# Performance work log

Measured on AMD Instinct MI355X. Metric: run time of the kernel, lower is better.

The kernel has to match this reference:

```python
import jax, jax.numpy as jnp
import numpy as np

NUM_CHANNELS = 64  # d per group
T_ITERS = 5
EPS = 1e-05


def setup_inputs() -> dict:
    key = jax.random.key(0)
    kx, = jax.random.split(key, 1)
    X = jax.random.normal(kx, (64, 256, 56, 56), dtype=jnp.float32)
    weight = jnp.ones((1, 256, 1, 1), dtype=jnp.float32)
    bias = jnp.zeros((1, 256, 1, 1), dtype=jnp.float32)
    return {"X": X, "weight": weight, "bias": bias}


def reference(X, weight, bias):
    B, C, H, W = X.shape
    nc = NUM_CHANNELS
    g = C // nc
    # (C, B, H, W) -> (g, nc, m) with m = B*H*W
    x = jnp.transpose(X, (1, 0, 2, 3)).reshape(g, nc, -1)
    m = x.shape[-1]
    mean = x.mean(-1, keepdims=True)                      # (g, nc, 1)
    xc = x - mean
    I = jnp.broadcast_to(jnp.eye(nc, dtype=X.dtype), (g, nc, nc))
    # Sigma = eps*I + (1/m) * xc @ xc^T
    Sigma = EPS * I + jnp.einsum('gdm,gem->gde', xc, xc) / m
    # rTr = 1 / trace(Sigma) per group
    rTr = (1.0 / jnp.einsum('gii->g', Sigma))[:, None, None]  # (g,1,1)
    Sigma_N = Sigma * rTr
    # Newton-Schulz iteration: P <- 1.5*P - 0.5*P^3 @ Sigma_N
    P = I
    for _ in range(T_ITERS):
        P3 = jnp.einsum('gij,gjk,gkl->gil', P, P, P)
        P = 1.5 * P - 0.5 * jnp.einsum('gij,gjk->gik', P3, Sigma_N)
    wm = P * jnp.sqrt(rTr)                                 # whitening matrix (g, nc, nc)
    xn = jnp.einsum('gde,gem->gdm', wm, xc)                # whitened data
    X_hat = jnp.transpose(xn.reshape(C, B, H, W), (1, 0, 2, 3))
    return X_hat * weight + bias
```

## Files before the change

kernel.cpp:

```cpp
#include <hip/hip_runtime.h>
#include <hip/hip_bf16.h>
#include <math.h>


#define EPS_F 1e-5f

using f32x4v = __attribute__((ext_vector_type(4))) float;
using f32x2v = __attribute__((ext_vector_type(2))) float;
using short8 = __attribute__((ext_vector_type(8))) short;
using u32x4  = __attribute__((ext_vector_type(4))) unsigned int;

constexpr int Cc  = 256;
constexpr int HWc = 3136;
constexpr int CHW = Cc * HWc;
constexpr float Mf = 200704.0f;
constexpr int GX  = 196;
constexpr int LDB = 72;

constexpr int WS_SUM  = 0;
constexpr int WS_G    = 256;
constexpr int WS_WM   = WS_G + 16384;
constexpr int WS_BETA = WS_WM + 16384;
constexpr int WS_SLAB = WS_BETA + 256;
constexpr int WS_SSUM = WS_SLAB + 784 * 4096;

__device__ __forceinline__ unsigned cvtpk(float lo, float hi) {
    __hip_bfloat162 h = __float22bfloat162_rn(float2{lo, hi});
    unsigned u;
    __builtin_memcpy(&u, &h, 4);
    return u;
}

__device__ __forceinline__ f32x4v mfma16(short8 a, short8 b, f32x4v c) {
    return __builtin_amdgcn_mfma_f32_16x16x32_bf16(a, b, c, 0, 0, 0);
}

extern "C" __global__ __launch_bounds__(256, 4)
void k_gram(const float* __restrict__ X, float* __restrict__ ws) {
    __shared__ __align__(16) unsigned short tg[2][2][64 * LDB];
    const int g = blockIdx.y, bx = blockIdx.x, tid = threadIdx.x;
    const int lane = tid & 63, w = tid >> 6;
    const int row = tid >> 2, mo = (tid & 3) << 4;
    const int l15 = lane & 15, lg = lane >> 4;
    const int CBi0 = (w >> 1) << 1, CBj0 = (w & 1) << 1;
    const float* Xg = X + (size_t)g * 64 * HWc;

    f32x4v acc[2][2];
    #pragma unroll
    for (int i = 0; i < 2; ++i)
        #pragma unroll
        for (int j = 0; j < 2; ++j) acc[i][j] = (f32x4v){0.f, 0.f, 0.f, 0.f};
    float csum = 0.0f;

    f32x4v curA[4], curB[4];
    auto loadt = [&](int t, f32x4v* cur) {
        const int b = t / 49, hw0 = (t - b * 49) << 6;
        const float* p = Xg + (size_t)b * CHW + (size_t)row * HWc + hw0 + mo;
        cur[0] = *(const f32x4v*)(p);      cur[1] = *(const f32x4v*)(p + 4);
        cur[2] = *(const f32x4v*)(p + 8);  cur[3] = *(const f32x4v*)(p + 12);
    };
    auto packt = [&](const f32x4v* cur, unsigned short* dstbuf) {
        unsigned pk[8];
        #pragma unroll
        for (int i = 0; i < 4; ++i) {
            csum += (cur[i].x + cur[i].y) + (cur[i].z + cur[i].w);
            pk[2*i]   = cvtpk(cur[i].x, cur[i].y);
            pk[2*i+1] = cvtpk(cur[i].z, cur[i].w);
        }
        unsigned short* dst = dstbuf + row * LDB + mo;
        *(u32x4*)(dst)     = (u32x4){pk[0], pk[1], pk[2], pk[3]};
        *(u32x4*)(dst + 8) = (u32x4){pk[4], pk[5], pk[6], pk[7]};
    };
    auto comp = [&](const unsigned short* T) {
        #pragma unroll
        for (int s = 0; s < 2; ++s) {
            const int ko = 8 * lg + 32 * s;
            const short8 a0 = *(const short8*)&T[(CBi0 * 16      + l15) * LDB + ko];
            const short8 a1 = *(const short8*)&T[((CBi0+1) * 16  + l15) * LDB + ko];
            const short8 b0 = *(const short8*)&T[(CBj0 * 16      + l15) * LDB + ko];
            const short8 b1 = *(const short8*)&T[((CBj0+1) * 16  + l15) * LDB + ko];
            acc[0][0] = mfma16(a0, b0, acc[0][0]);
            acc[0][1] = mfma16(a0, b1, acc[0][1]);
            acc[1][0] = mfma16(a1, b0, acc[1][0]);
            acc[1][1] = mfma16(a1, b1, acc[1][1]);
        }
    };

    loadt(bx, curA);
    loadt(bx + GX, curB);

    int buf = 0;
    for (int kk = 0; kk < 8; ++kk) {
        packt(curA, tg[buf][0]);
        packt(curB, tg[buf][1]);
        __syncthreads();
        if (kk < 7) {
            loadt(bx + GX * (2*kk + 2), curA);
            loadt(bx + GX * (2*kk + 3), curB);
        }
        comp(tg[buf][0]);
        comp(tg[buf][1]);
        buf ^= 1;
    }

    csum += __shfl_down(csum, 1, 4);
    csum += __shfl_down(csum, 2, 4);
    if ((tid & 3) == 0)
        ws[WS_SSUM + (g * GX + bx) * 64 + row] = csum;

    float* Gp = ws + WS_SLAB + (size_t)(g * GX + bx) * 4096;
    #pragma unroll
    for (int ci = 0; ci < 2; ++ci)
        #pragma unroll
        for (int cj = 0; cj < 2; ++cj)
            #pragma unroll
            for (int reg = 0; reg < 4; ++reg) {
                const int r = (CBi0 + ci) * 16 + lg * 4 + reg;
                const int c = (CBj0 + cj) * 16 + l15;
                Gp[r * 64 + c] = acc[ci][cj][reg];
            }
}

extern "C" __global__ __launch_bounds__(256)
void k_reduce(float* __restrict__ ws) {
    const int g = blockIdx.y, chunk = blockIdx.x, tid = threadIdx.x;
    const int cell = chunk * 256 + tid;
    const float* p = ws + WS_SLAB + (size_t)g * GX * 4096 + cell;
    float s0 = 0.f, s1 = 0.f, s2 = 0.f, s3 = 0.f;
    #pragma unroll 7
    for (int s4 = 0; s4 < 49; ++s4) {
        s0 += p[0];
        s1 += p[4096];
        s2 += p[2 * 4096];
        s3 += p[3 * 4096];
        p += 4 * 4096;
    }
    ws[WS_G + g * 4096 + cell] = (s0 + s1) + (s2 + s3);

    if (chunk == 0 && tid < 64) {
        const float* q = ws + WS_SSUM + (size_t)g * GX * 64 + tid;
        float a0 = 0.f, a1 = 0.f, a2 = 0.f, a3 = 0.f;
        #pragma unroll 7
        for (int s4 = 0; s4 < 49; ++s4) {
            a0 += q[0];
            a1 += q[64];
            a2 += q[128];
            a3 += q[192];
            q += 256;
        }
        ws[WS_SUM + g * 64 + tid] = (a0 + a1) + (a2 + a3);
    }
}

__device__ __forceinline__
void mm64s(float* C, const float* A, const float* B, int r0, int c0) {
    f32x4v s[4] = {{0,0,0,0},{0,0,0,0},{0,0,0,0},{0,0,0,0}};
    #pragma unroll 4
    for (int kk = 0; kk < 16; ++kk) {
        const f32x4v b0 = *(const f32x4v*)&B[(4*kk + 0) * 68 + c0];
        const f32x4v b1 = *(const f32x4v*)&B[(4*kk + 1) * 68 + c0];
        const f32x4v b2 = *(const f32x4v*)&B[(4*kk + 2) * 68 + c0];
        const f32x4v b3 = *(const f32x4v*)&B[(4*kk + 3) * 68 + c0];
        #pragma unroll
        for (int i = 0; i < 4; ++i) {
            const f32x4v a = *(const f32x4v*)&A[(r0 + i) * 68 + 4 * kk];
            s[i] += a.x * b0 + a.y * b1 + a.z * b2 + a.w * b3;
        }
    }
    __syncthreads();
    #pragma unroll
    for (int i = 0; i < 4; ++i) *(f32x4v*)&C[(r0 + i) * 68 + c0] = s[i];
    __syncthreads();
}

extern "C" __global__ __launch_bounds__(256)
void k_solve(const float* __restrict__ weight, const float* __restrict__ bias,
             float* __restrict__ ws) {
    __shared__ __align__(16) float M [64 * 68];
    __shared__ __align__(16) float P [64 * 68];
    __shared__ __align__(16) float W [64 * 68];
    __shared__ __align__(16) float T1[64 * 68];
    __shared__ __align__(16) float mean_s[64];
    __shared__ float red;

    const int g = blockIdx.x, tid = threadIdx.x;
    const int r = tid >> 2, ch = (tid & 3) << 4;
    const int r0 = (tid >> 4) << 2, c0 = (tid & 15) << 2;

    if (tid < 64) mean_s[tid] = ws[WS_SUM + g * 64 + tid] * (1.0f / Mf);
    __syncthreads();

    const float* Gp = ws + WS_G + g * 4096;
    const float mr = mean_s[r];
    #pragma unroll
    for (int j4 = 0; j4 < 4; ++j4) {
        const int c = ch + 4 * j4;
        const f32x4v gv = *(const f32x4v*)&Gp[r * 64 + c];
        const f32x4v mc = *(const f32x4v*)&mean_s[c];
        f32x4v sv, pv = {0,0,0,0};
        #pragma unroll
        for (int j = 0; j < 4; ++j) {
            float v = gv[j] * (1.0f / Mf) - mr * mc[j];
            if (c + j == r) { v += EPS_F; pv[j] = 1.0f; }
            sv[j] = v;
        }
        *(f32x4v*)&M[r * 68 + c] = sv;
        *(f32x4v*)&P[r * 68 + c] = pv;
    }
    __syncthreads();

    if (tid == 0) {
        float tr = 0.f;
        #pragma unroll
        for (int i = 0; i < 64; ++i) tr += M[i * 68 + i];
        red = 1.0f / tr;
    }
    __syncthreads();
    const float rtr = red;
    #pragma unroll
    for (int j4 = 0; j4 < 4; ++j4) {
        const int c = ch + 4 * j4;
        *(f32x4v*)&M[r * 68 + c] = *(const f32x4v*)&M[r * 68 + c] * rtr;
    }
    __syncthreads();

    for (int t = 0; t < 5; ++t) {
        #pragma unroll
        for (int j4 = 0; j4 < 4; ++j4) {
            const int c = ch + 4 * j4;
            f32x4v mv = *(const f32x4v*)&M[r * 68 + c];
            f32x4v wv = -0.5f * mv;
            #pragma unroll
            for (int j = 0; j < 4; ++j) if (c + j == r) wv[j] += 1.5f;
            *(f32x4v*)&W[r * 68 + c] = wv;
        }
        __syncthreads();
        mm64s(P, P, W, r0, c0);
        if (t < 4) {
            mm64s(T1, M, W, r0, c0);
            mm64s(M, T1, W, r0, c0);
        }
    }

    const float srtr = sqrtf(rtr);
    const float wr = weight[g * 64 + r];
    float* Wp = ws + WS_WM + g * 4096;
    float part = 0.0f;
    #pragma unroll
    for (int j4 = 0; j4 < 4; ++j4) {
        const int c = ch + 4 * j4;
        const f32x4v pv = *(const f32x4v*)&P[r * 68 + c] * srtr;
        *(f32x4v*)&Wp[r * 64 + c] = pv * wr;
        const f32x4v mc = *(const f32x4v*)&mean_s[c];
        part += pv.x * mc.x + pv.y * mc.y + pv.z * mc.z + pv.w * mc.w;
    }
    part += __shfl_down(part, 1, 4);
    part += __shfl_down(part, 2, 4);
    if ((tid & 3) == 0)
        ws[WS_BETA + g * 64 + r] = bias[g * 64 + r] - wr * part;
}

extern "C" __global__ __launch_bounds__(256, 4)
void k_apply(const float* __restrict__ X, const float* __restrict__ ws,
             float* __restrict__ out) {
    __shared__ __align__(16) unsigned short tx[2][2][64 * LDB];
    __shared__ __align__(16) float beta_sh[64];

    const int g = blockIdx.y, bx = blockIdx.x, tid = threadIdx.x;
    const int lane = tid & 63, w = tid >> 6;
    const int l15 = lane & 15, lg = lane >> 4;
    const float* Xg = X + (size_t)g * 64 * HWc;

    {
        unsigned short* wm_s = &tx[0][0][0];
        const float* Wp = ws + WS_WM + g * 4096;
        const int r = tid >> 2, ch = (tid & 3) << 4;
        const float* p = Wp + r * 64 + ch;
        const f32x4v v0 = *(const f32x4v*)(p);      const f32x4v v1 = *(const f32x4v*)(p + 4);
        const f32x4v v2 = *(const f32x4v*)(p + 8);  const f32x4v v3 = *(const f32x4v*)(p + 12);
        unsigned short* dst = &wm_s[r * LDB + ch];
        *(u32x4*)(dst)     = (u32x4){cvtpk(v0.x,v0.y), cvtpk(v0.z,v0.w),
                                     cvtpk(v1.x,v1.y), cvtpk(v1.z,v1.w)};
        *(u32x4*)(dst + 8) = (u32x4){cvtpk(v2.x,v2.y), cvtpk(v2.z,v2.w),
                                     cvtpk(v3.x,v3.y), cvtpk(v3.z,v3.w)};
        if (tid < 64) beta_sh[tid] = ws[WS_BETA + g * 64 + tid];
    }
    __syncthreads();

    const int CB0 = (w >> 1) << 1, MB0 = (w & 1) << 1;
    short8 afrag[2][2];
    {
        const unsigned short* wm_s = &tx[0][0][0];
        #pragma unroll
        for (int ci = 0; ci < 2; ++ci)
            #pragma unroll
            for (int s = 0; s < 2; ++s)
                afrag[ci][s] = *(const short8*)&wm_s[((CB0 + ci) * 16 + l15) * LDB + 8 * lg + 32 * s];
    }

    float betav[2][4]; int crow[2][4];
    #pragma unroll
    for (int ci = 0; ci < 2; ++ci)
        #pragma unroll
        for (int reg = 0; reg < 4; ++reg) {
            const int cl = (CB0 + ci) * 16 + lg * 4 + reg;
            betav[ci][reg] = beta_sh[cl];
            crow[ci][reg]  = (g * 64 + cl) * HWc;
        }
    __syncthreads();

    const int rT   = 32 * (lane >> 5) + 16 * (lane & 1) + ((lane & 31) >> 1);
    const int mcb  = 32 * (w & 1) + 2 * l15;
    const int e0 = w * 16;

    float curA[16], curB[16];
    auto loadt = [&](int t, float* cur) {
        const int b = t / 49, hw0 = (t - b * 49) << 6;
        const float* p = Xg + (size_t)b * CHW + (size_t)e0 * HWc + hw0 + lane;
        #pragma unroll
        for (int j = 0; j < 16; ++j) cur[j] = p[(size_t)j * HWc];
    };
    auto packt = [&](const float* cur, unsigned short* dstbuf) {
        unsigned short* dst = dstbuf + rT * LDB + e0;
        *(u32x4*)(dst)     = (u32x4){cvtpk(cur[0],cur[1]),   cvtpk(cur[2],cur[3]),
                                     cvtpk(cur[4],cur[5]),   cvtpk(cur[6],cur[7])};
        *(u32x4*)(dst + 8) = (u32x4){cvtpk(cur[8],cur[9]),   cvtpk(cur[10],cur[11]),
                                     cvtpk(cur[12],cur[13]), cvtpk(cur[14],cur[15])};
    };
    auto compst = [&](const unsigned short* T, int t) {
        f32x4v acc[2][2];
        #pragma unroll
        for (int i = 0; i < 2; ++i)
            #pragma unroll
            for (int j = 0; j < 2; ++j) acc[i][j] = (f32x4v){0.f,0.f,0.f,0.f};
        #pragma unroll
        for (int s = 0; s < 2; ++s) {
            const int ko = 8 * lg + 32 * s;
            const short8 b0 = *(const short8*)&T[(MB0 * 16     + l15) * LDB + ko];
            const short8 b1 = *(const short8*)&T[((MB0+1) * 16 + l15) * LDB + ko];
            acc[0][0] = mfma16(afrag[0][s], b0, acc[0][0]);
            acc[0][1] = mfma16(afrag[0][s], b1, acc[0][1]);
            acc[1][0] = mfma16(afrag[1][s], b0, acc[1][0]);
            acc[1][1] = mfma16(afrag[1][s], b1, acc[1][1]);
        }
        const int b = t / 49, hw0 = (t - b * 49) << 6;
        float* ob = out + (size_t)b * CHW + hw0 + mcb;
        #pragma unroll
        for (int ci = 0; ci < 2; ++ci)
            #pragma unroll
            for (int reg = 0; reg < 4; ++reg) {
                const float bt = betav[ci][reg];
                const f32x2v v = {acc[ci][0][reg] + bt, acc[ci][1][reg] + bt};
                __builtin_nontemporal_store(v, (f32x2v*)(ob + crow[ci][reg]));
            }
    };

    loadt(bx, curA);
    loadt(bx + GX, curB);

    int buf = 0;
    for (int kk = 0; kk < 8; ++kk) {
        packt(curA, tx[buf][0]);
        packt(curB, tx[buf][1]);
        __syncthreads();
        if (kk < 7) {
            loadt(bx + GX * (2*kk + 2), curA);
            loadt(bx + GX * (2*kk + 3), curB);
        }
        compst(tx[buf][0], bx + GX * (2*kk));
        compst(tx[buf][1], bx + GX * (2*kk + 1));
        buf ^= 1;
    }
}

extern "C" void kernel_launch(void* const* d_in, const int* in_sizes, int n_in,
                              void* d_out, int out_size, void* d_ws, size_t ws_size,
                              hipStream_t stream) {
    const float* X      = (const float*)d_in[0];
    const float* weight = (const float*)d_in[1];
    const float* bias   = (const float*)d_in[2];
    float* out = (float*)d_out;
    float* ws  = (float*)d_ws;

    hipLaunchKernelGGL(k_gram,   dim3(GX, 4), dim3(256), 0, stream, X, ws);
    hipLaunchKernelGGL(k_reduce, dim3(16, 4), dim3(256), 0, stream, ws);
    hipLaunchKernelGGL(k_solve,  dim3(4),     dim3(256), 0, stream, weight, bias, ws);
    hipLaunchKernelGGL(k_apply,  dim3(GX, 4), dim3(256), 0, stream, X, ws, out);
}
```

Measured before the change: 153.5 us.

## Use split-bf16 MFMA for Newton-Schulz solve and widen slab reduction grid

The 64x64 fp32 matrix products in the Newton-Schulz solve were done with scalar FMAs from shared memory. They now run on bf16 MFMA instructions, with each operand split into high and low bf16 parts and three products summed to keep near-fp32 accuracy. Separately, the slab reduction now uses 4x more blocks, each splitting the 196 partial slabs across four waves and combining the results in shared memory. The goal is to cut the serial latency of the tiny single-block-per-group solve kernel and to give the reduction more parallelism. The cost is extra precision-splitting and conversion work, and slightly less accuracy than true fp32.

```diff
diff --git a/kernel.cpp b/kernel.cpp
--- a/kernel.cpp
+++ b/kernel.cpp
@@ -29,6 +29,16 @@
     unsigned u;
     __builtin_memcpy(&u, &h, 4);
     return u;
+}
+
+__device__ __forceinline__ unsigned short bf16rn(float v) {
+    unsigned u = __builtin_bit_cast(unsigned, v);
+    u += 0x7FFFu + ((u >> 16) & 1u);
+    return (unsigned short)(u >> 16);
+}
+__device__ __forceinline__ float frombf(unsigned short h) {
+    unsigned u = (unsigned)h << 16;
+    return __builtin_bit_cast(float, u);
 }
 
 __device__ __forceinline__ f32x4v mfma16(short8 a, short8 b, f32x4v c) {
@@ -123,122 +133,175 @@
 
 extern "C" __global__ __launch_bounds__(256)
 void k_reduce(float* __restrict__ ws) {
+    __shared__ float part[4][64];
     const int g = blockIdx.y, chunk = blockIdx.x, tid = threadIdx.x;
-    const int cell = chunk * 256 + tid;
-    const float* p = ws + WS_SLAB + (size_t)g * GX * 4096 + cell;
-    float s0 = 0.f, s1 = 0.f, s2 = 0.f, s3 = 0.f;
+    const int c63 = tid & 63, q = tid >> 6;
+    const float* p = ws + WS_SLAB + (size_t)g * GX * 4096
+                   + (size_t)(q * 49) * 4096 + chunk * 64 + c63;
+    float s = 0.f;
     #pragma unroll 7
-    for (int s4 = 0; s4 < 49; ++s4) {
-        s0 += p[0];
-        s1 += p[4096];
-        s2 += p[2 * 4096];
-        s3 += p[3 * 4096];
-        p += 4 * 4096;
-    }
-    ws[WS_G + g * 4096 + cell] = (s0 + s1) + (s2 + s3);
+    for (int i = 0; i < 49; ++i) { s += *p; p += 4096; }
+    part[q][c63] = s;
+    __syncthreads();
+    if (tid < 64)
+        ws[WS_G + g * 4096 + chunk * 64 + tid] =
+            (part[0][tid] + part[1][tid]) + (part[2][tid] + part[3][tid]);
 
     if (chunk == 0 && tid < 64) {
-        const float* q = ws + WS_SSUM + (size_t)g * GX * 64 + tid;
+        const float* qq = ws + WS_SSUM + (size_t)g * GX * 64 + tid;
         float a0 = 0.f, a1 = 0.f, a2 = 0.f, a3 = 0.f;
         #pragma unroll 7
         for (int s4 = 0; s4 < 49; ++s4) {
-            a0 += q[0];
-            a1 += q[64];
-            a2 += q[128];
-            a3 += q[192];
-            q += 256;
+            a0 += qq[0];
+            a1 += qq[64];
+            a2 += qq[128];
+            a3 += qq[192];
+            qq += 256;
         }
         ws[WS_SUM + g * 64 + tid] = (a0 + a1) + (a2 + a3);
     }
 }
 
-__device__ __forceinline__
-void mm64s(float* C, const float* A, const float* B, int r0, int c0) {
-    f32x4v s[4] = {{0,0,0,0},{0,0,0,0},{0,0,0,0},{0,0,0,0}};
-    #pragma unroll 4
-    for (int kk = 0; kk < 16; ++kk) {
-        const f32x4v b0 = *(const f32x4v*)&B[(4*kk + 0) * 68 + c0];
-        const f32x4v b1 = *(const f32x4v*)&B[(4*kk + 1) * 68 + c0];
-        const f32x4v b2 = *(const f32x4v*)&B[(4*kk + 2) * 68 + c0];
-        const f32x4v b3 = *(const f32x4v*)&B[(4*kk + 3) * 68 + c0];
-        #pragma unroll
-        for (int i = 0; i < 4; ++i) {
-            const f32x4v a = *(const f32x4v*)&A[(r0 + i) * 68 + 4 * kk];
-            s[i] += a.x * b0 + a.y * b1 + a.z * b2 + a.w * b3;
-        }
-    }
-    __syncthreads();
-    #pragma unroll
-    for (int i = 0; i < 4; ++i) *(f32x4v*)&C[(r0 + i) * 68 + c0] = s[i];
+__device__ __forceinline__ void mm_bf(
+    unsigned short* Ch, unsigned short* Cl,
+    const unsigned short* Ah, const unsigned short* Al,
+    const unsigned short* Bh, const unsigned short* Bl,
+    int CBi0, int CBj0, int l15, int lg)
+{
+    short8 ah[2][2], al[2][2];
+    #pragma unroll
+    for (int ci = 0; ci < 2; ++ci)
+        #pragma unroll
+        for (int s = 0; s < 2; ++s) {
+            const int off = ((CBi0 + ci) * 16 + l15) * LDB + 8 * lg + 32 * s;
+            ah[ci][s] = *(const short8*)&Ah[off];
+            al[ci][s] = *(const short8*)&Al[off];
+        }
+    __syncthreads();
+
+    f32x4v acc[2][2];
+    #pragma unroll
+    for (int i = 0; i < 2; ++i)
+        #pragma unroll
+        for (int j = 0; j < 2; ++j) acc[i][j] = (f32x4v){0.f, 0.f, 0.f, 0.f};
+
+    #pragma unroll
+    for (int s = 0; s < 2; ++s) {
+        short8 bh[2], bl[2];
+        #pragma unroll
+        for (int cj = 0; cj < 2; ++cj) {
+            const int off = ((CBj0 + cj) * 16 + l15) * LDB + 8 * lg + 32 * s;
+            bh[cj] = *(const short8*)&Bh[off];
+            bl[cj] = *(const short8*)&Bl[off];
+        }
+        #pragma unroll
+        for (int ci = 0; ci < 2; ++ci)
+            #pragma unroll
+            for (int cj = 0; cj < 2; ++cj)
+                acc[ci][cj] = mfma16(ah[ci][s], bh[cj], acc[ci][cj]);
+        #pragma unroll
+        for (int ci = 0; ci < 2; ++ci)
+            #pragma unroll
+            for (int cj = 0; cj < 2; ++cj)
+                acc[ci][cj] = mfma16(al[ci][s], bh[cj], acc[ci][cj]);
+        #pragma unroll
+        for (int ci = 0; ci < 2; ++ci)
+            #pragma unroll
+            for (int cj = 0; cj < 2; ++cj)
+                acc[ci][cj] = mfma16(ah[ci][s], bl[cj], acc[ci][cj]);
+    }
+
+    #pragma unroll
+    for (int ci = 0; ci < 2; ++ci)
+        #pragma unroll
+        for (int cj = 0; cj < 2; ++cj)
+            #pragma unroll
+            for (int reg = 0; reg < 4; ++reg) {
+                const int row = (CBi0 + ci) * 16 + lg * 4 + reg;
+                const int col = (CBj0 + cj) * 16 + l15;
+                const float c = acc[ci][cj][reg];
+                const unsigned short h = bf16rn(c);
+                Ch[row * LDB + col] = h;
+                Cl[row * LDB + col] = bf16rn(c - frombf(h));
+            }
     __syncthreads();
 }
 
 extern "C" __global__ __launch_bounds__(256)
 void k_solve(const float* __restrict__ weight, const float* __restrict__ bias,
              float* __restrict__ ws) {
-    __shared__ __align__(16) float M [64 * 68];
-    __shared__ __align__(16) float P [64 * 68];
-    __shared__ __align__(16) float W [64 * 68];
-    __shared__ __align__(16) float T1[64 * 68];
-    __shared__ __align__(16) float mean_s[64];
+    __shared__ __align__(16) unsigned short Mh[64 * LDB], Ml[64 * LDB];
+    __shared__ __align__(16) unsigned short Ph[64 * LDB], Pl[64 * LDB];
+    __shared__ __align__(16) unsigned short Wh[64 * LDB], Wl[64 * LDB];
+    __shared__ __align__(16) unsigned short Th[64 * LDB], Tl[64 * LDB];
+    __shared__ float mean_s[64];
+    __shared__ float diag_s[64];
     __shared__ float red;
 
     const int g = blockIdx.x, tid = threadIdx.x;
+    const int lane = tid & 63, w = tid >> 6;
+    const int l15 = lane & 15, lg = lane >> 4;
+    const int CBi0 = (w >> 1) << 1, CBj0 = (w & 1) << 1;
     const int r = tid >> 2, ch = (tid & 3) << 4;
-    const int r0 = (tid >> 4) << 2, c0 = (tid & 15) << 2;
 
     if (tid < 64) mean_s[tid] = ws[WS_SUM + g * 64 + tid] * (1.0f / Mf);
     __syncthreads();
 
     const float* Gp = ws + WS_G + g * 4096;
     const float mr = mean_s[r];
+    f32x4v sv[4];
     #pragma unroll
     for (int j4 = 0; j4 < 4; ++j4) {
         const int c = ch + 4 * j4;
         const f32x4v gv = *(const f32x4v*)&Gp[r * 64 + c];
         const f32x4v mc = *(const f32x4v*)&mean_s[c];
-        f32x4v sv, pv = {0,0,0,0};
         #pragma unroll
         for (int j = 0; j < 4; ++j) {
             float v = gv[j] * (1.0f / Mf) - mr * mc[j];
-            if (c + j == r) { v += EPS_F; pv[j] = 1.0f; }
-            sv[j] = v;
-        }
-        *(f32x4v*)&M[r * 68 + c] = sv;
-        *(f32x4v*)&P[r * 68 + c] = pv;
-    }
-    __syncthreads();
-
+            if (c + j == r) { v += EPS_F; diag_s[r] = v; }
+            sv[j4][j] = v;
+        }
+    }
+    __syncthreads();
     if (tid == 0) {
         float tr = 0.f;
         #pragma unroll
-        for (int i = 0; i < 64; ++i) tr += M[i * 68 + i];
+        for (int i = 0; i < 64; ++i) tr += diag_s[i];
         red = 1.0f / tr;
     }
     __syncthreads();
     const float rtr = red;
+
     #pragma unroll
     for (int j4 = 0; j4 < 4; ++j4) {
-        const int c = ch + 4 * j4;
-        *(f32x4v*)&M[r * 68 + c] = *(const f32x4v*)&M[r * 68 + c] * rtr;
+        #pragma unroll
+        for (int j = 0; j < 4; ++j) {
+            const int c = ch + 4 * j4 + j;
+            const float v = sv[j4][j] * rtr;
+            const unsigned short h = bf16rn(v);
+            Mh[r * LDB + c] = h;
+            Ml[r * LDB + c] = bf16rn(v - frombf(h));
+            Ph[r * LDB + c] = (c == r) ? (unsigned short)0x3F80 : (unsigned short)0;
+            Pl[r * LDB + c] = 0;
+        }
     }
     __syncthreads();
 
     for (int t = 0; t < 5; ++t) {
         #pragma unroll
-        for (int j4 = 0; j4 < 4; ++j4) {
-            const int c = ch + 4 * j4;
-            f32x4v mv = *(const f32x4v*)&M[r * 68 + c];
-            f32x4v wv = -0.5f * mv;
-            #pragma unroll
-            for (int j = 0; j < 4; ++j) if (c + j == r) wv[j] += 1.5f;
-            *(f32x4v*)&W[r * 68 + c] = wv;
+        for (int j16 = 0; j16 < 16; ++j16) {
+            const int c = ch + j16;
+            const float m = frombf(Mh[r * LDB + c]) + frombf(Ml[r * LDB + c]);
+            const float wv = ((c == r) ? 1.5f : 0.0f) - 0.5f * m;
+            const unsigned short h = bf16rn(wv);
+            Wh[r * LDB + c] = h;
+            Wl[r * LDB + c] = bf16rn(wv - frombf(h));
         }
         __syncthreads();
-        mm64s(P, P, W, r0, c0);
+        mm_bf(Ph, Pl, Ph, Pl, Wh, Wl, CBi0, CBj0, l15, lg);
         if (t < 4) {
-            mm64s(T1, M, W, r0, c0);
-            mm64s(M, T1, W, r0, c0);
+            mm_bf(Th, Tl, Mh, Ml, Wh, Wl, CBi0, CBj0, l15, lg);
+            mm_bf(Mh, Ml, Th, Tl, Wh, Wl, CBi0, CBj0, l15, lg);
         }
     }
 
@@ -247,12 +310,12 @@
     float* Wp = ws + WS_WM + g * 4096;
     float part = 0.0f;
     #pragma unroll
-    for (int j4 = 0; j4 < 4; ++j4) {
-        const int c = ch + 4 * j4;
-        const f32x4v pv = *(const f32x4v*)&P[r * 68 + c] * srtr;
-        *(f32x4v*)&Wp[r * 64 + c] = pv * wr;
-        const f32x4v mc = *(const f32x4v*)&mean_s[c];
-        part += pv.x * mc.x + pv.y * mc.y + pv.z * mc.z + pv.w * mc.w;
+    for (int j16 = 0; j16 < 16; ++j16) {
+        const int c = ch + j16;
+        const float p = frombf(Ph[r * LDB + c]) + frombf(Pl[r * LDB + c]);
+        const float wm = p * srtr;
+        Wp[r * 64 + c] = wm * wr;
+        part += wm * mean_s[c];
     }
     part += __shfl_down(part, 1, 4);
     part += __shfl_down(part, 2, 4);
@@ -274,11 +337,11 @@
     {
         unsigned short* wm_s = &tx[0][0][0];
         const float* Wp = ws + WS_WM + g * 4096;
-        const int r = tid >> 2, ch = (tid & 3) << 4;
-        const float* p = Wp + r * 64 + ch;
+        const int r = tid >> 2, chh = (tid & 3) << 4;
+        const float* p = Wp + r * 64 + chh;
         const f32x4v v0 = *(const f32x4v*)(p);      const f32x4v v1 = *(const f32x4v*)(p + 4);
         const f32x4v v2 = *(const f32x4v*)(p + 8);  const f32x4v v3 = *(const f32x4v*)(p + 12);
-        unsigned short* dst = &wm_s[r * LDB + ch];
+        unsigned short* dst = &wm_s[r * LDB + chh];
         *(u32x4*)(dst)     = (u32x4){cvtpk(v0.x,v0.y), cvtpk(v0.z,v0.w),
                                      cvtpk(v1.x,v1.y), cvtpk(v1.z,v1.w)};
         *(u32x4*)(dst + 8) = (u32x4){cvtpk(v2.x,v2.y), cvtpk(v2.z,v2.w),
@@ -383,7 +446,7 @@
     float* ws  = (float*)d_ws;
 
     hipLaunchKernelGGL(k_gram,   dim3(GX, 4), dim3(256), 0, stream, X, ws);
-    hipLaunchKernelGGL(k_reduce, dim3(16, 4), dim3(256), 0, stream, ws);
+    hipLaunchKernelGGL(k_reduce, dim3(64, 4), dim3(256), 0, stream, ws);
     hipLaunchKernelGGL(k_solve,  dim3(4),     dim3(256), 0, stream, weight, bias, ws);
     hipLaunchKernelGGL(k_apply,  dim3(GX, 4), dim3(256), 0, stream, X, ws, out);
 }
```

New measurement: 133.4 us. -13.1%, faster.
